# Performance work log

Hardware: AMD Instinct MI355X
Metric: run time of the kernel (lower is better)

The kernel has to match this reference:

```python
import jax, jax.numpy as jnp
import numpy as np

B, L, H = 4, 1024, 1024
NH, HD = 16, 64
ND = NH * HD
ITERS = 4
U = 5  # MSA1 ring window size (hard-coded in source)


def _conv1x1(w, b, x):  # w [O,C], b [O], x [B,C,L] -> [B,O,L]  (Conv2d 1x1 == per-position linear)
    return jnp.einsum('oc,bcl->bol', w, x) + b[None, :, None]


def _layernorm(x, s, b, eps=1e-5):  # x [B,H,L]; LayerNorm over channel dim H
    mu = x.mean(1, keepdims=True)
    var = ((x - mu) ** 2).mean(1, keepdims=True)
    return (x - mu) / jnp.sqrt(var + eps) * s[None, :, None] + b[None, :, None]


def _msa1(x, ax, wq, bq, wk, bk, wv, bv, wo, bo):
    # x [B,H,L] normalized nodes; ax [B,H,2,L] (ring embedding + relay)
    b, h, l = x.shape
    q = _conv1x1(wq, bq, x).reshape(b, NH, HD, l)
    k = _conv1x1(wk, bk, x).reshape(b, NH, HD, l)
    v = _conv1x1(wv, bv, x).reshape(b, NH, HD, l)
    pad = U // 2
    kp = jnp.pad(k, ((0, 0), (0, 0), (0, 0), (pad, pad)))
    vp = jnp.pad(v, ((0, 0), (0, 0), (0, 0), (pad, pad)))
    # F.unfold with (U,1) kernel along L == stack of U shifted views
    kw = jnp.stack([kp[..., u:u + l] for u in range(U)], axis=3)  # [B,NH,HD,U,L]
    vw = jnp.stack([vp[..., u:u + l] for u in range(U)], axis=3)
    al = ax.shape[2]
    ak = (jnp.einsum('oc,bcal->boal', wk, ax) + bk[None, :, None, None]).reshape(b, NH, HD, al, l)
    av = (jnp.einsum('oc,bcal->boal', wv, ax) + bv[None, :, None, None]).reshape(b, NH, HD, al, l)
    kw = jnp.concatenate([kw, ak], axis=3)  # [B,NH,HD,U+2,L]
    vw = jnp.concatenate([vw, av], axis=3)
    scores = (q[:, :, :, None, :] * kw).sum(2) / np.sqrt(HD)  # [B,NH,U+2,L]
    alphas = jax.nn.softmax(scores, axis=2)
    att = (alphas[:, :, None, :, :] * vw).sum(3).reshape(b, ND, l)
    return _conv1x1(wo, bo, att)  # [B,H,L]


def _msa2(relay, y, smask, wq, bq, wk, bk, wo, bo):
    # relay [B,H]; y [B,H,L+1]; smask [B,L+1] True at padding
    b = relay.shape[0]
    q = (jnp.einsum('oc,bc->bo', wq, relay) + bq).reshape(b, NH, HD)
    k = _conv1x1(wk, bk, y).reshape(b, NH, HD, -1)
    pre = jnp.einsum('bnd,bndl->bnl', q, k) / np.sqrt(HD)
    pre = jnp.where(smask[:, None, :], -1e10, pre)
    alphas = jax.nn.softmax(pre, axis=-1)
    # NOTE: source has v = k (WV output unused) -- reproduced faithfully
    att = jnp.einsum('bnl,bndl->bnd', alphas, k).reshape(b, ND)
    return jnp.einsum('oc,bc->bo', wo, att) + bo  # [B,H]


def _star_forward(data, mask, ln_s, ln_b, rwq, rwq_b, rwk, rwk_b, rwv, rwv_b, rwo, rwo_b,
                  swq, swq_b, swk, swk_b, swo, swo_b):
    b, l, h = data.shape
    pad_mask = (mask == 0)  # True at padding positions
    smask = jnp.concatenate([jnp.zeros((b, 1), bool), pad_mask], axis=1)  # [B,L+1]
    embs = jnp.transpose(data, (0, 2, 1))  # [B,H,L]
    nodes = embs
    relay = embs.mean(2)  # [B,H]
    for i in range(ITERS):
        xn = _layernorm(nodes, ln_s[i], ln_b[i])
        ax = jnp.stack([embs, jnp.broadcast_to(relay[:, :, None], embs.shape)], axis=2)  # [B,H,2,L]
        ring = _msa1(xn, ax, rwq[i], rwq_b[i], rwk[i], rwk_b[i], rwv[i], rwv_b[i], rwo[i], rwo_b[i])
        nodes = nodes + jax.nn.leaky_relu(ring)
        y = jnp.concatenate([relay[:, :, None], nodes], axis=2)  # [B,H,L+1]
        relay = jax.nn.leaky_relu(_msa2(relay, y, smask, swq[i], swq_b[i], swk[i], swk_b[i], swo[i], swo_b[i]))
        nodes = jnp.where(pad_mask[:, None, :], 0.0, nodes)
    return jnp.transpose(nodes, (0, 2, 1)), relay  # [B,L,H], [B,H]


def setup_inputs() -> dict:
    key = jax.random.key(0)
    ks = jax.random.split(key, 16)
    def p(k, shape):
        return jax.random.normal(k, shape, jnp.float32) * 0.02
    return dict(
        data=jax.random.normal(ks[0], (B, L, H), jnp.float32),
        mask=jax.random.randint(ks[1], (B, L), 0, 2).astype(jnp.int32),
        ln_s=jnp.ones((ITERS, H), jnp.float32),
        ln_b=jnp.zeros((ITERS, H), jnp.float32),
        rwq=p(ks[2], (ITERS, ND, H)), rwq_b=p(ks[3], (ITERS, ND)),
        rwk=p(ks[4], (ITERS, ND, H)), rwk_b=p(ks[5], (ITERS, ND)),
        rwv=p(ks[6], (ITERS, ND, H)), rwv_b=p(ks[7], (ITERS, ND)),
        rwo=p(ks[8], (ITERS, H, ND)), rwo_b=p(ks[9], (ITERS, H)),
        swq=p(ks[10], (ITERS, ND, H)), swq_b=p(ks[11], (ITERS, ND)),
        swk=p(ks[12], (ITERS, ND, H)), swk_b=p(ks[13], (ITERS, ND)),
        swo=p(ks[14], (ITERS, H, ND)), swo_b=p(ks[15], (ITERS, H)),
    )


def reference(data, mask, ln_s, ln_b, rwq, rwq_b, rwk, rwk_b, rwv, rwv_b, rwo, rwo_b,
              swq, swq_b, swk, swk_b, swo, swo_b):
    return _star_forward(data, mask, ln_s, ln_b, rwq, rwq_b, rwk, rwk_b, rwv, rwv_b,
                         rwo, rwo_b, swq, swq_b, swk, swk_b, swo, swo_b)
```

## Files before the change

kernel.cpp:

```cpp
#include <hip/hip_runtime.h>
#include <math.h>

namespace {

constexpr int B_ = 4, L_ = 1024, H_ = 1024, NH_ = 16, HD_ = 64, ND_ = 1024, ITERS_ = 4;

typedef unsigned short u16;
typedef __attribute__((ext_vector_type(8))) short short8;
typedef __attribute__((ext_vector_type(4))) float f32x4;

__device__ inline u16 f2bf(float f) {
  unsigned u = __builtin_bit_cast(unsigned, f);
  u += 0x7FFFu + ((u >> 16) & 1u);
  return (u16)(u >> 16);
}
__device__ inline float bf2f(u16 v) {
  unsigned u = ((unsigned)v) << 16;
  return __builtin_bit_cast(float, u);
}

__device__ inline void gl_lds16(const u16* g, u16* l) {
  __builtin_amdgcn_global_load_lds((const __attribute__((address_space(1))) void*)g,
                                   (__attribute__((address_space(3))) void*)l, 16, 0, 0);
}

__global__ void k_prep(const float* __restrict__ data, const float* __restrict__ rwq,
                       const float* __restrict__ rwk, const float* __restrict__ rwv,
                       const float* __restrict__ rwo, const float* __restrict__ swk,
                       u16* __restrict__ embs_bf, u16* __restrict__ wq_bf,
                       u16* __restrict__ wk_bf, u16* __restrict__ wv_bf,
                       u16* __restrict__ wo_bf, u16* __restrict__ swk_bf,
                       float* __restrict__ nodes) {
  int i = blockIdx.x * 256 + threadIdx.x;
  int which = blockIdx.y;
  if (which == 6) {
    reinterpret_cast<float4*>(nodes)[i] = reinterpret_cast<const float4*>(data)[i];
    return;
  }
  const float* src;
  u16* dst;
  switch (which) {
    case 0: src = data; dst = embs_bf; break;
    case 1: src = rwq; dst = wq_bf; break;
    case 2: src = rwk; dst = wk_bf; break;
    case 3: src = rwv; dst = wv_bf; break;
    case 4: src = rwo; dst = wo_bf; break;
    default: src = swk; dst = swk_bf; break;
  }
  float4 v = reinterpret_cast<const float4*>(src)[i];
  ushort4 o;
  o.x = f2bf(v.x); o.y = f2bf(v.y); o.z = f2bf(v.z); o.w = f2bf(v.w);
  reinterpret_cast<ushort4*>(dst)[i] = o;
}

__global__ void k_relay_part(const float* __restrict__ data, float* __restrict__ part) {
  int b = blockIdx.z, chunk = blockIdx.y;
  int c = blockIdx.x * 256 + threadIdx.x;
  const float* p = data + ((size_t)b * L_ + chunk * 128) * H_ + c;
  float acc = 0.f;
  for (int l = 0; l < 128; ++l) acc += p[(size_t)l * H_];
  part[((size_t)b * 8 + chunk) * H_ + c] = acc;
}
__global__ void k_relay_reduce(const float* __restrict__ part, float* __restrict__ relay) {
  int i = blockIdx.x * 256 + threadIdx.x;
  int b = i >> 10, c = i & 1023;
  float acc = 0.f;
  for (int j = 0; j < 8; ++j) acc += part[((size_t)b * 8 + j) * H_ + c];
  relay[i] = acc * (1.f / (float)L_);
}

__global__ __launch_bounds__(256) void k_layernorm_bf(float* __restrict__ nodes,
                                                      const float* __restrict__ s,
                                                      const float* __restrict__ bb,
                                                      const int* __restrict__ mask,
                                                      u16* __restrict__ y, int do_zero) {
  int row = blockIdx.x * 4 + (threadIdx.x >> 6);
  int lane = threadIdx.x & 63;
  int b = row >> 10, l = row & 1023;
  bool pad = do_zero && (mask[b * L_ + l] == 0);
  float4* xr = reinterpret_cast<float4*>(nodes + (size_t)row * H_);
  float4 v[4];
  float sum = 0.f, sq = 0.f;
#pragma unroll
  for (int j = 0; j < 4; ++j) {
    v[j] = pad ? float4{0.f, 0.f, 0.f, 0.f} : xr[lane + 64 * j];
    sum += v[j].x + v[j].y + v[j].z + v[j].w;
    sq += v[j].x * v[j].x + v[j].y * v[j].y + v[j].z * v[j].z + v[j].w * v[j].w;
  }
  if (pad) {
#pragma unroll
    for (int j = 0; j < 4; ++j) xr[lane + 64 * j] = float4{0.f, 0.f, 0.f, 0.f};
  }
#pragma unroll
  for (int off = 32; off; off >>= 1) {
    sum += __shfl_xor(sum, off);
    sq += __shfl_xor(sq, off);
  }
  float mu = sum * (1.f / (float)H_);
  float rstd = rsqrtf(sq * (1.f / (float)H_) - mu * mu + 1e-5f);
  ushort4* yr = reinterpret_cast<ushort4*>(y + (size_t)row * H_);
#pragma unroll
  for (int j = 0; j < 4; ++j) {
    int c4 = lane + 64 * j;
    float4 sc = reinterpret_cast<const float4*>(s)[c4];
    float4 bc = reinterpret_cast<const float4*>(bb)[c4];
    ushort4 o;
    o.x = f2bf((v[j].x - mu) * rstd * sc.x + bc.x);
    o.y = f2bf((v[j].y - mu) * rstd * sc.y + bc.y);
    o.z = f2bf((v[j].z - mu) * rstd * sc.z + bc.z);
    o.w = f2bf((v[j].w - mu) * rstd * sc.w + bc.w);
    yr[c4] = o;
  }
}


#define GEMM_PROLOGUE(XPTR, WPTR)                                              \
  __shared__ __align__(16) u16 sX[128 * 32];                                   \
  __shared__ __align__(16) u16 sW[128 * 32];                                   \
  const int t = threadIdx.x;                                                   \
  const int w = t >> 6, lane = t & 63;                                         \
  const int wm = w >> 1, wn = w & 1;                                           \
  const int r4 = lane >> 2, slot = lane & 3;                                   \
  const int rowS0 = w * 16 + r4, rowS1 = 64 + rowS0;                           \
  const int colS0 = ((slot ^ ((rowS0 >> 1) & 3)) << 3);                        \
  const int colS1 = ((slot ^ ((rowS1 >> 1) & 3)) << 3);                        \
  const u16* gX0 = (XPTR) + (size_t)(bm + rowS0) * 1024 + colS0;               \
  const u16* gX1 = (XPTR) + (size_t)(bm + rowS1) * 1024 + colS1;               \
  const u16* gW0 = (WPTR) + (size_t)(bn + rowS0) * 1024 + colS0;               \
  const u16* gW1 = (WPTR) + (size_t)(bn + rowS1) * 1024 + colS1;               \
  u16* lX0 = sX + (size_t)w * 512;                                             \
  u16* lX1 = sX + (size_t)(4 + w) * 512;                                       \
  u16* lW0 = sW + (size_t)w * 512;                                             \
  u16* lW1 = sW + (size_t)(4 + w) * 512;                                       \
  const int kidx = (((lane >> 4) ^ ((lane >> 1) & 3)) << 3);                   \
  f32x4 acc[4][4];                                                             \
  _Pragma("unroll") for (int i_ = 0; i_ < 4; ++i_)                             \
      _Pragma("unroll") for (int j_ = 0; j_ < 4; ++j_)                         \
          acc[i_][j_] = f32x4{0.f, 0.f, 0.f, 0.f};

#define GEMM_KLOOP(AROWBASE, BROWBASE, ASRC, BSRC)                             \
  for (int ck = 0; ck < 1024; ck += 32) {                                      \
    gl_lds16(gX0, lX0);                                                        \
    gl_lds16(gX1, lX1);                                                        \
    gl_lds16(gW0, lW0);                                                        \
    gl_lds16(gW1, lW1);                                                        \
    gX0 += 32; gX1 += 32; gW0 += 32; gW1 += 32;                                \
    __syncthreads();                                                           \
    short8 af_[4], bf_[4];                                                     \
    _Pragma("unroll") for (int mf = 0; mf < 4; ++mf)                           \
        af_[mf] = *reinterpret_cast<const short8*>(                            \
            &ASRC[((AROWBASE) + mf * 16) * 32 + kidx]);                        \
    _Pragma("unroll") for (int nf = 0; nf < 4; ++nf)                           \
        bf_[nf] = *reinterpret_cast<const short8*>(                            \
            &BSRC[((BROWBASE) + nf * 16) * 32 + kidx]);                        \
    _Pragma("unroll") for (int mf = 0; mf < 4; ++mf)                           \
        _Pragma("unroll") for (int nf = 0; nf < 4; ++nf)                       \
            acc[mf][nf] = __builtin_amdgcn_mfma_f32_16x16x32_bf16(             \
                af_[mf], bf_[nf], acc[mf][nf], 0, 0, 0);                       \
    __syncthreads();                                                          \
  }

__global__ __launch_bounds__(256) void k_gemm5(const u16* __restrict__ wq,
                                               const u16* __restrict__ wk,
                                               const u16* __restrict__ wv,
                                               const float* __restrict__ bq,
                                               const float* __restrict__ bk,
                                               const float* __restrict__ bv,
                                               const u16* __restrict__ xn,
                                               const u16* __restrict__ embs,
                                               u16* __restrict__ Y) {
  const int bm = blockIdx.x * 128;
  const int which = blockIdx.y >> 3;
  const int bn = (blockIdx.y & 7) * 128;
  const u16* W = (which == 0) ? wq : ((which == 1 || which == 3) ? wk : wv);
  const float* bias = (which == 0) ? bq : ((which == 1 || which == 3) ? bk : bv);
  const u16* X = (which < 3) ? xn : embs;
  u16* Yw = Y + (size_t)which * ((size_t)B_ * L_ * ND_);

  GEMM_PROLOGUE(X, W)
  const int rW = wm * 64 + (lane & 15);
  const int rX = wn * 64 + (lane & 15);
  GEMM_KLOOP(rW, rX, sW, sX)

#pragma unroll
  for (int mo = 0; mo < 4; ++mo) {
    int o0 = bn + wm * 64 + mo * 16 + ((lane >> 4) << 2);
    float4 bs = *reinterpret_cast<const float4*>(bias + o0);
#pragma unroll
    for (int nl = 0; nl < 4; ++nl) {
      int bl = bm + wn * 64 + nl * 16 + (lane & 15);
      f32x4 vv = acc[mo][nl];
      ushort4 ov;
      ov.x = f2bf(vv[0] + bs.x);
      ov.y = f2bf(vv[1] + bs.y);
      ov.z = f2bf(vv[2] + bs.z);
      ov.w = f2bf(vv[3] + bs.w);
      *reinterpret_cast<ushort4*>(&Yw[(size_t)bl * 1024 + o0]) = ov;
    }
  }
}

__global__ __launch_bounds__(256) void k_gemm_wo(const u16* __restrict__ W,
                                                 const float* __restrict__ bias,
                                                 const u16* __restrict__ X,
                                                 float* __restrict__ nodes,
                                                 u16* __restrict__ nodes_bf) {
  const int bm = blockIdx.x * 128;
  const int bn = blockIdx.y * 128;
  GEMM_PROLOGUE(X, W)
  const int rW = wm * 64 + (lane & 15);
  const int rX = wn * 64 + (lane & 15);
  GEMM_KLOOP(rW, rX, sW, sX)

#pragma unroll
  for (int mo = 0; mo < 4; ++mo) {
    int o0 = bn + wm * 64 + mo * 16 + ((lane >> 4) << 2);
    float4 bs = *reinterpret_cast<const float4*>(bias + o0);
#pragma unroll
    for (int nl = 0; nl < 4; ++nl) {
      int bl = bm + wn * 64 + nl * 16 + (lane & 15);
      size_t ni = (size_t)bl * 1024 + o0;
      float4 cur = *reinterpret_cast<const float4*>(&nodes[ni]);
      f32x4 vv = acc[mo][nl];
      float r0 = vv[0] + bs.x; r0 = cur.x + (r0 > 0.f ? r0 : 0.01f * r0);
      float r1 = vv[1] + bs.y; r1 = cur.y + (r1 > 0.f ? r1 : 0.01f * r1);
      float r2 = vv[2] + bs.z; r2 = cur.z + (r2 > 0.f ? r2 : 0.01f * r2);
      float r3 = vv[3] + bs.w; r3 = cur.w + (r3 > 0.f ? r3 : 0.01f * r3);
      *reinterpret_cast<float4*>(&nodes[ni]) = float4{r0, r1, r2, r3};
      ushort4 ov;
      ov.x = f2bf(r0); ov.y = f2bf(r1); ov.z = f2bf(r2); ov.w = f2bf(r3);
      *reinterpret_cast<ushort4*>(&nodes_bf[ni]) = ov;
    }
  }
}

__global__ __launch_bounds__(256) void k_gemm_kkb(const u16* __restrict__ W,
                                                  const float* __restrict__ bias,
                                                  const u16* __restrict__ X,
                                                  float* __restrict__ Y) {
  const int bm = blockIdx.x * 128;
  const int bn = blockIdx.y * 128;
  GEMM_PROLOGUE(X, W)
  const int rX = wm * 64 + (lane & 15);
  const int rW = wn * 64 + (lane & 15);
  GEMM_KLOOP(rX, rW, sX, sW)

#pragma unroll
  for (int nf = 0; nf < 4; ++nf) {
    int o = bn + wn * 64 + nf * 16 + (lane & 15);
    float bs = bias[o];
#pragma unroll
    for (int mf = 0; mf < 4; ++mf) {
      int gl = bm + wm * 64 + mf * 16 + ((lane >> 4) << 2);
      int b = gl >> 10, l = gl & 1023;
      size_t yi = ((size_t)(b * 1024 + o)) * (size_t)(L_ + 1) + 1 + l;
      f32x4 v = acc[mf][nf];
#pragma unroll
      for (int r = 0; r < 4; ++r) Y[yi + r] = v[r] + bs;
    }
  }
}

__global__ __launch_bounds__(256) void k_matvec2(const float* __restrict__ W0,
                                                 const float* __restrict__ b0,
                                                 float* __restrict__ y0, long sB0, long sO0,
                                                 const float* __restrict__ W1,
                                                 const float* __restrict__ b1,
                                                 float* __restrict__ y1, long sB1, long sO1,
                                                 const float* __restrict__ x) {
  int b = blockIdx.y;
  int z = blockIdx.z;
  const float* W = z ? W1 : W0;
  const float* bias = z ? b1 : b0;
  float* y = z ? y1 : y0;
  long sB = z ? sB1 : sB0, sO = z ? sO1 : sO0;
  int o = blockIdx.x * 4 + (threadIdx.x >> 6);
  int lane = threadIdx.x & 63;
  const float* wr = W + (size_t)o * 1024;
  const float* xb = x + (size_t)b * 1024;
  float acc = 0.f;
  for (int c = lane; c < 1024; c += 64) acc += wr[c] * xb[c];
#pragma unroll
  for (int off = 32; off; off >>= 1) acc += __shfl_xor(acc, off);
  if (lane == 0) y[(size_t)b * sB + (size_t)o * sO] = acc + bias[o];
}

__global__ __launch_bounds__(256) void k_matvec(const float* __restrict__ W,
                                                const float* __restrict__ bias,
                                                const float* __restrict__ x,
                                                float* __restrict__ y) {
  int b = blockIdx.y;
  int o = blockIdx.x * 4 + (threadIdx.x >> 6);
  int lane = threadIdx.x & 63;
  const float* wr = W + (size_t)o * 1024;
  const float* xb = x + (size_t)b * 1024;
  float acc = 0.f;
  for (int c = lane; c < 1024; c += 64) acc += wr[c] * xb[c];
#pragma unroll
  for (int off = 32; off; off >>= 1) acc += __shfl_xor(acc, off);
  if (lane == 0) {
    acc += bias[o];
    y[(size_t)b * 1024 + o] = acc > 0.f ? acc : 0.01f * acc;
  }
}

__global__ __launch_bounds__(256) void k_msa1(const u16* __restrict__ q,
                                              const u16* __restrict__ k,
                                              const u16* __restrict__ v,
                                              const u16* __restrict__ ke,
                                              const u16* __restrict__ ve,
                                              const float* __restrict__ rk,
                                              const float* __restrict__ rv,
                                              u16* __restrict__ attbf) {
  int t = threadIdx.x;
  int head = t & 15, dh = (t >> 4) & 1, lsub = t >> 5;
  int l = blockIdx.x * 8 + lsub;
  int b = blockIdx.z;
  size_t row = ((size_t)(b * 1024 + l)) * 1024 + head * 64 + dh * 32;
  size_t rbase = (size_t)b * 1024 + head * 64 + dh * 32;

  float qf[32];
  {
    const short8* qp = reinterpret_cast<const short8*>(q + row);
#pragma unroll
    for (int j = 0; j < 4; ++j) {
      short8 qv = qp[j];
#pragma unroll
      for (int e = 0; e < 8; ++e) qf[j * 8 + e] = bf2f((u16)qv[e]);
    }
  }
  float s[7];
#pragma unroll
  for (int u = 0; u < 5; ++u) {
    int lk = l + u - 2;
    float su = 0.f;
    if (lk >= 0 && lk < L_) {
      const short8* kp =
          reinterpret_cast<const short8*>(k + ((size_t)(b * 1024 + lk)) * 1024 + head * 64 + dh * 32);
#pragma unroll
      for (int j = 0; j < 4; ++j) {
        short8 kv = kp[j];
#pragma unroll
        for (int e = 0; e < 8; ++e) su = fmaf(qf[j * 8 + e], bf2f((u16)kv[e]), su);
      }
    }
    s[u] = su;
  }
  {
    float su = 0.f;
    const short8* kp = reinterpret_cast<const short8*>(ke + row);
#pragma unroll
    for (int j = 0; j < 4; ++j) {
      short8 kv = kp[j];
#pragma unroll
      for (int e = 0; e < 8; ++e) su = fmaf(qf[j * 8 + e], bf2f((u16)kv[e]), su);
    }
    s[5] = su;
  }
  {
    float su = 0.f;
    const float4* rp = reinterpret_cast<const float4*>(rk + rbase);
#pragma unroll
    for (int j = 0; j < 8; ++j) {
      float4 r4 = rp[j];
      su = fmaf(qf[j * 4 + 0], r4.x, su);
      su = fmaf(qf[j * 4 + 1], r4.y, su);
      su = fmaf(qf[j * 4 + 2], r4.z, su);
      su = fmaf(qf[j * 4 + 3], r4.w, su);
    }
    s[6] = su;
  }
#pragma unroll
  for (int u = 0; u < 7; ++u) s[u] += __shfl_xor(s[u], 16);
  float m = -1e30f;
#pragma unroll
  for (int u = 0; u < 7; ++u) {
    s[u] *= 0.125f;
    m = fmaxf(m, s[u]);
  }
  float e[7], tot = 0.f;
#pragma unroll
  for (int u = 0; u < 7; ++u) {
    e[u] = expf(s[u] - m);
    tot += e[u];
  }
  float inv = 1.f / tot;
#pragma unroll
  for (int u = 0; u < 7; ++u) e[u] *= inv;

  float av[32];
  {
    const float4* rp = reinterpret_cast<const float4*>(rv + rbase);
#pragma unroll
    for (int j = 0; j < 8; ++j) {
      float4 r4 = rp[j];
      av[j * 4 + 0] = e[6] * r4.x;
      av[j * 4 + 1] = e[6] * r4.y;
      av[j * 4 + 2] = e[6] * r4.z;
      av[j * 4 + 3] = e[6] * r4.w;
    }
  }
  {
    const short8* vp = reinterpret_cast<const short8*>(ve + row);
#pragma unroll
    for (int j = 0; j < 4; ++j) {
      short8 vv = vp[j];
#pragma unroll
      for (int ee = 0; ee < 8; ++ee) av[j * 8 + ee] = fmaf(e[5], bf2f((u16)vv[ee]), av[j * 8 + ee]);
    }
  }
#pragma unroll
  for (int u = 0; u < 5; ++u) {
    int lk = l + u - 2;
    if (lk >= 0 && lk < L_) {
      const short8* vp =
          reinterpret_cast<const short8*>(v + ((size_t)(b * 1024 + lk)) * 1024 + head * 64 + dh * 32);
#pragma unroll
      for (int j = 0; j < 4; ++j) {
        short8 vv = vp[j];
#pragma unroll
        for (int ee = 0; ee < 8; ++ee) av[j * 8 + ee] = fmaf(e[u], bf2f((u16)vv[ee]), av[j * 8 + ee]);
      }
    }
  }
  u16 ob[32];
#pragma unroll
  for (int j = 0; j < 32; ++j) ob[j] = f2bf(av[j]);
  uint4* d4 = reinterpret_cast<uint4*>(attbf + row);
  const uint4* s4 = reinterpret_cast<const uint4*>(ob);
#pragma unroll
  for (int j = 0; j < 4; ++j) d4[j] = s4[j];
}

__global__ __launch_bounds__(1024) void k_msa2(const float* __restrict__ rq,
                                               const float* __restrict__ kk,
                                               const int* __restrict__ mask,
                                               float* __restrict__ satt) {
  int n = blockIdx.x, b = blockIdx.y;
  int t = threadIdx.x;
  __shared__ float sq_[HD_];
  __shared__ float se[L_ + 1];
  __shared__ float swsum[16];
  __shared__ float stot;
  size_t rb = (size_t)(b * NH_ + n) * HD_;
  if (t < HD_) sq_[t] = rq[rb + t];
  __syncthreads();
  const float* kb = kk + rb * (size_t)(L_ + 1);
  float ls = 0.f;
  for (int p = t; p < L_ + 1; p += 1024) {
    float e;
    if (p > 0 && mask[b * L_ + p - 1] == 0) {
      e = 0.f;
    } else {
      float acc = 0.f;
      for (int d = 0; d < HD_; ++d) acc = fmaf(sq_[d], kb[(size_t)d * (L_ + 1) + p], acc);
      e = expf(acc * 0.125f);
    }
    se[p] = e;
    ls += e;
  }
  int lane = t & 63, w = t >> 6;
#pragma unroll
  for (int off = 32; off; off >>= 1) ls += __shfl_xor(ls, off);
  if (lane == 0) swsum[w] = ls;
  __syncthreads();
  if (t == 0) {
    float tot = 0.f;
    for (int j = 0; j < 16; ++j) tot += swsum[j];
    stot = 1.f / tot;
  }
  __syncthreads();
  float inv = stot;
  float acc[4] = {0.f, 0.f, 0.f, 0.f};
  const float* kw = kb + (size_t)(w * 4) * (L_ + 1);
  for (int p = lane; p < L_ + 1; p += 64) {
    float e = se[p];
#pragma unroll
    for (int j = 0; j < 4; ++j) acc[j] = fmaf(e, kw[(size_t)j * (L_ + 1) + p], acc[j]);
  }
#pragma unroll
  for (int j = 0; j < 4; ++j) {
    float a = acc[j];
#pragma unroll
    for (int off = 32; off; off >>= 1) a += __shfl_xor(a, off);
    if (lane == 0) satt[rb + w * 4 + j] = a * inv;
  }
}

__global__ void k_final(const float* __restrict__ nodes, const int* __restrict__ mask,
                        float* __restrict__ out) {
  int i = blockIdx.x * 256 + threadIdx.x;
  int row = i >> 8;
  int b = row >> 10, l = row & 1023;
  float4 v = (mask[b * L_ + l] == 0) ? float4{0.f, 0.f, 0.f, 0.f}
                                     : reinterpret_cast<const float4*>(nodes)[i];
  reinterpret_cast<float4*>(out)[i] = v;
}

__global__ void k_copy_relay(const float* __restrict__ relay, float* __restrict__ out) {
  int i = blockIdx.x * 256 + threadIdx.x;
  out[i] = relay[i];
}

}

extern "C" void kernel_launch(void* const* d_in, const int* in_sizes, int n_in,
                              void* d_out, int out_size, void* d_ws, size_t ws_size,
                              hipStream_t stream) {
  (void)in_sizes; (void)n_in; (void)out_size; (void)ws_size;
  const float* data = (const float*)d_in[0];
  const int* mask = (const int*)d_in[1];
  const float* ln_s = (const float*)d_in[2];
  const float* ln_b = (const float*)d_in[3];
  const float* rwq = (const float*)d_in[4];
  const float* rwq_b = (const float*)d_in[5];
  const float* rwk = (const float*)d_in[6];
  const float* rwk_b = (const float*)d_in[7];
  const float* rwv = (const float*)d_in[8];
  const float* rwv_b = (const float*)d_in[9];
  const float* rwo = (const float*)d_in[10];
  const float* rwo_b = (const float*)d_in[11];
  const float* swq = (const float*)d_in[12];
  const float* swq_b = (const float*)d_in[13];
  const float* swk = (const float*)d_in[14];
  const float* swk_b = (const float*)d_in[15];
  const float* swo = (const float*)d_in[16];
  const float* swo_b = (const float*)d_in[17];
  float* out = (float*)d_out;

  const size_t SZ = (size_t)B_ * ND_ * L_;
  float* f = (float*)d_ws;
  float* nodes = f; f += SZ;
  float* kkb = f; f += (size_t)B_ * ND_ * (L_ + 1);
  float* part = f; f += (size_t)B_ * 8 * H_;
  float* relay = f; f += B_ * H_;
  float* rk = f; f += B_ * ND_;
  float* rv = f; f += B_ * ND_;
  float* rq = f; f += B_ * ND_;
  float* satt = f; f += B_ * ND_;
  u16* u = (u16*)f;
  u16* xn_bf = u; u += SZ;
  u16* embs_bf = u; u += SZ;
  u16* att_bf = u; u += SZ;
  u16* nodes_bf = u; u += SZ;
  u16* qkv5_bf = u; u += 5 * SZ;
  u16* wq_bf = u; u += SZ;
  u16* wk_bf = u; u += SZ;
  u16* wv_bf = u; u += SZ;
  u16* wo_bf = u; u += SZ;
  u16* swk_bf = u; u += SZ;

  k_prep<<<dim3(4096, 7), 256, 0, stream>>>(data, rwq, rwk, rwv, rwo, swk,
                                            embs_bf, wq_bf, wk_bf, wv_bf, wo_bf, swk_bf, nodes);
  k_relay_part<<<dim3(H_ / 256, 8, B_), 256, 0, stream>>>(data, part);
  k_relay_reduce<<<dim3((B_ * H_) / 256), 256, 0, stream>>>(part, relay);

  for (int i = 0; i < ITERS_; ++i) {
    const u16* wq_i = wq_bf + (size_t)i * ND_ * H_;
    const u16* wk_i = wk_bf + (size_t)i * ND_ * H_;
    const u16* wv_i = wv_bf + (size_t)i * ND_ * H_;
    const u16* wo_i = wo_bf + (size_t)i * H_ * ND_;
    const u16* sk_i = swk_bf + (size_t)i * ND_ * H_;

    k_layernorm_bf<<<dim3(B_ * L_ / 4), 256, 0, stream>>>(nodes, ln_s + i * H_, ln_b + i * H_,
                                                          mask, xn_bf, i > 0 ? 1 : 0);
    k_gemm5<<<dim3(32, 40), 256, 0, stream>>>(wq_i, wk_i, wv_i,
                                              rwq_b + i * ND_, rwk_b + i * ND_, rwv_b + i * ND_,
                                              xn_bf, embs_bf, qkv5_bf);
    k_matvec2<<<dim3(256, B_, 2), 256, 0, stream>>>(
        rwk + (size_t)i * ND_ * H_, rwk_b + i * ND_, rk, ND_, 1,
        rwv + (size_t)i * ND_ * H_, rwv_b + i * ND_, rv, ND_, 1, relay);
    k_msa1<<<dim3(L_ / 8, 1, B_), 256, 0, stream>>>(qkv5_bf, qkv5_bf + SZ, qkv5_bf + 2 * SZ,
                                                    qkv5_bf + 3 * SZ, qkv5_bf + 4 * SZ, rk, rv, att_bf);
    k_gemm_wo<<<dim3(32, 8), 256, 0, stream>>>(wo_i, rwo_b + i * H_, att_bf, nodes, nodes_bf);
    k_matvec2<<<dim3(256, B_, 2), 256, 0, stream>>>(
        swq + (size_t)i * ND_ * H_, swq_b + i * ND_, rq, ND_, 1,
        swk + (size_t)i * ND_ * H_, swk_b + i * ND_, kkb, (long)ND_ * (L_ + 1), L_ + 1, relay);
    k_gemm_kkb<<<dim3(32, 8), 256, 0, stream>>>(sk_i, swk_b + i * ND_, nodes_bf, kkb);
    k_msa2<<<dim3(NH_, B_), 1024, 0, stream>>>(rq, kkb, mask, satt);
    k_matvec<<<dim3(256, B_), 256, 0, stream>>>(swo + (size_t)i * H_ * ND_, swo_b + i * H_, satt, relay);
  }
  k_final<<<4096, 256, 0, stream>>>(nodes, mask, out);
  k_copy_relay<<<dim3((B_ * H_) / 256), 256, 0, stream>>>(relay, out + (size_t)B_ * L_ * H_);
}
```

Baseline: 767.8 us.

## Reassociate MSA2 through WK, double K-step GEMMs, and remap MSA1 threads

MSA2 no longer materializes K = WK·nodes for all positions. It folds the query into WK (qt = WKᵀq), scores positions directly against the bf16 nodes, forms an exp-weighted sum of the nodes, and then applies WK once per head. This removes the per-iteration 1024x1024x4096 K-projection GEMM and the large kkb buffer, in exchange for several small matvec, score and sum kernels and a change in rounding order. Separately, the GEMM K loop now loads 64-wide chunks into two LDS buffers per barrier pair with a 3-block occupancy hint, and MSA1 uses 4 lanes per head so each thread holds fewer registers.

```diff
diff --git a/kernel.cpp b/kernel.cpp
--- a/kernel.cpp
+++ b/kernel.cpp
@@ -26,14 +26,13 @@
 
 __global__ void k_prep(const float* __restrict__ data, const float* __restrict__ rwq,
                        const float* __restrict__ rwk, const float* __restrict__ rwv,
-                       const float* __restrict__ rwo, const float* __restrict__ swk,
+                       const float* __restrict__ rwo,
                        u16* __restrict__ embs_bf, u16* __restrict__ wq_bf,
                        u16* __restrict__ wk_bf, u16* __restrict__ wv_bf,
-                       u16* __restrict__ wo_bf, u16* __restrict__ swk_bf,
-                       float* __restrict__ nodes) {
+                       u16* __restrict__ wo_bf, float* __restrict__ nodes) {
   int i = blockIdx.x * 256 + threadIdx.x;
   int which = blockIdx.y;
-  if (which == 6) {
+  if (which == 5) {
     reinterpret_cast<float4*>(nodes)[i] = reinterpret_cast<const float4*>(data)[i];
     return;
   }
@@ -44,8 +43,7 @@
     case 1: src = rwq; dst = wq_bf; break;
     case 2: src = rwk; dst = wk_bf; break;
     case 3: src = rwv; dst = wv_bf; break;
-    case 4: src = rwo; dst = wo_bf; break;
-    default: src = swk; dst = swk_bf; break;
+    default: src = rwo; dst = wo_bf; break;
   }
   float4 v = reinterpret_cast<const float4*>(src)[i];
   ushort4 o;
@@ -115,8 +113,8 @@
 
 
 #define GEMM_PROLOGUE(XPTR, WPTR)                                              \
-  __shared__ __align__(16) u16 sX[128 * 32];                                   \
-  __shared__ __align__(16) u16 sW[128 * 32];                                   \
+  __shared__ __align__(16) u16 sX[2][128 * 32];                                \
+  __shared__ __align__(16) u16 sW[2][128 * 32];                                \
   const int t = threadIdx.x;                                                   \
   const int w = t >> 6, lane = t & 63;                                         \
   const int wm = w >> 1, wn = w & 1;                                           \
@@ -128,47 +126,57 @@
   const u16* gX1 = (XPTR) + (size_t)(bm + rowS1) * 1024 + colS1;               \
   const u16* gW0 = (WPTR) + (size_t)(bn + rowS0) * 1024 + colS0;               \
   const u16* gW1 = (WPTR) + (size_t)(bn + rowS1) * 1024 + colS1;               \
-  u16* lX0 = sX + (size_t)w * 512;                                             \
-  u16* lX1 = sX + (size_t)(4 + w) * 512;                                       \
-  u16* lW0 = sW + (size_t)w * 512;                                             \
-  u16* lW1 = sW + (size_t)(4 + w) * 512;                                       \
+  u16* lX0a = sX[0] + w * 512;                                                 \
+  u16* lX0b = sX[1] + w * 512;                                                 \
+  u16* lX1a = sX[0] + (4 + w) * 512;                                           \
+  u16* lX1b = sX[1] + (4 + w) * 512;                                           \
+  u16* lW0a = sW[0] + w * 512;                                                 \
+  u16* lW0b = sW[1] + w * 512;                                                 \
+  u16* lW1a = sW[0] + (4 + w) * 512;                                           \
+  u16* lW1b = sW[1] + (4 + w) * 512;                                           \
   const int kidx = (((lane >> 4) ^ ((lane >> 1) & 3)) << 3);                   \
   f32x4 acc[4][4];                                                             \
   _Pragma("unroll") for (int i_ = 0; i_ < 4; ++i_)                             \
       _Pragma("unroll") for (int j_ = 0; j_ < 4; ++j_)                         \
           acc[i_][j_] = f32x4{0.f, 0.f, 0.f, 0.f};
 
-#define GEMM_KLOOP(AROWBASE, BROWBASE, ASRC, BSRC)                             \
-  for (int ck = 0; ck < 1024; ck += 32) {                                      \
-    gl_lds16(gX0, lX0);                                                        \
-    gl_lds16(gX1, lX1);                                                        \
-    gl_lds16(gW0, lW0);                                                        \
-    gl_lds16(gW1, lW1);                                                        \
-    gX0 += 32; gX1 += 32; gW0 += 32; gW1 += 32;                                \
+#define GEMM_KLOOP64(AROWBASE, BROWBASE, ASRC, BSRC)                           \
+  for (int ck = 0; ck < 1024; ck += 64) {                                      \
+    gl_lds16(gX0, lX0a);                                                       \
+    gl_lds16(gX0 + 32, lX0b);                                                  \
+    gl_lds16(gX1, lX1a);                                                       \
+    gl_lds16(gX1 + 32, lX1b);                                                  \
+    gl_lds16(gW0, lW0a);                                                       \
+    gl_lds16(gW0 + 32, lW0b);                                                  \
+    gl_lds16(gW1, lW1a);                                                       \
+    gl_lds16(gW1 + 32, lW1b);                                                  \
+    gX0 += 64; gX1 += 64; gW0 += 64; gW1 += 64;                                \
     __syncthreads();                                                           \
-    short8 af_[4], bf_[4];                                                     \
-    _Pragma("unroll") for (int mf = 0; mf < 4; ++mf)                           \
-        af_[mf] = *reinterpret_cast<const short8*>(                            \
-            &ASRC[((AROWBASE) + mf * 16) * 32 + kidx]);                        \
-    _Pragma("unroll") for (int nf = 0; nf < 4; ++nf)                           \
-        bf_[nf] = *reinterpret_cast<const short8*>(                            \
-            &BSRC[((BROWBASE) + nf * 16) * 32 + kidx]);                        \
-    _Pragma("unroll") for (int mf = 0; mf < 4; ++mf)                           \
-        _Pragma("unroll") for (int nf = 0; nf < 4; ++nf)                       \
-            acc[mf][nf] = __builtin_amdgcn_mfma_f32_16x16x32_bf16(             \
-                af_[mf], bf_[nf], acc[mf][nf], 0, 0, 0);                       \
-    __syncthreads();                                                          \
-  }
-
-__global__ __launch_bounds__(256) void k_gemm5(const u16* __restrict__ wq,
-                                               const u16* __restrict__ wk,
-                                               const u16* __restrict__ wv,
-                                               const float* __restrict__ bq,
-                                               const float* __restrict__ bk,
-                                               const float* __restrict__ bv,
-                                               const u16* __restrict__ xn,
-                                               const u16* __restrict__ embs,
-                                               u16* __restrict__ Y) {
+    _Pragma("unroll") for (int h = 0; h < 2; ++h) {                            \
+      short8 af_[4], bf_[4];                                                   \
+      _Pragma("unroll") for (int mf = 0; mf < 4; ++mf)                         \
+          af_[mf] = *reinterpret_cast<const short8*>(                          \
+              &ASRC[h][((AROWBASE) + mf * 16) * 32 + kidx]);                   \
+      _Pragma("unroll") for (int nf = 0; nf < 4; ++nf)                         \
+          bf_[nf] = *reinterpret_cast<const short8*>(                          \
+              &BSRC[h][((BROWBASE) + nf * 16) * 32 + kidx]);                   \
+      _Pragma("unroll") for (int mf = 0; mf < 4; ++mf)                         \
+          _Pragma("unroll") for (int nf = 0; nf < 4; ++nf)                     \
+              acc[mf][nf] = __builtin_amdgcn_mfma_f32_16x16x32_bf16(           \
+                  af_[mf], bf_[nf], acc[mf][nf], 0, 0, 0);                     \
+    }                                                                          \
+    __syncthreads();                                                           \
+  }
+
+__global__ __launch_bounds__(256, 3) void k_gemm5(const u16* __restrict__ wq,
+                                                  const u16* __restrict__ wk,
+                                                  const u16* __restrict__ wv,
+                                                  const float* __restrict__ bq,
+                                                  const float* __restrict__ bk,
+                                                  const float* __restrict__ bv,
+                                                  const u16* __restrict__ xn,
+                                                  const u16* __restrict__ embs,
+                                                  u16* __restrict__ Y) {
   const int bm = blockIdx.x * 128;
   const int which = blockIdx.y >> 3;
   const int bn = (blockIdx.y & 7) * 128;
@@ -180,7 +188,7 @@
   GEMM_PROLOGUE(X, W)
   const int rW = wm * 64 + (lane & 15);
   const int rX = wn * 64 + (lane & 15);
-  GEMM_KLOOP(rW, rX, sW, sX)
+  GEMM_KLOOP64(rW, rX, sW, sX)
 
 #pragma unroll
   for (int mo = 0; mo < 4; ++mo) {
@@ -200,17 +208,17 @@
   }
 }
 
-__global__ __launch_bounds__(256) void k_gemm_wo(const u16* __restrict__ W,
-                                                 const float* __restrict__ bias,
-                                                 const u16* __restrict__ X,
-                                                 float* __restrict__ nodes,
-                                                 u16* __restrict__ nodes_bf) {
+__global__ __launch_bounds__(256, 3) void k_gemm_wo(const u16* __restrict__ W,
+                                                    const float* __restrict__ bias,
+                                                    const u16* __restrict__ X,
+                                                    float* __restrict__ nodes,
+                                                    u16* __restrict__ nodes_bf) {
   const int bm = blockIdx.x * 128;
   const int bn = blockIdx.y * 128;
   GEMM_PROLOGUE(X, W)
   const int rW = wm * 64 + (lane & 15);
   const int rX = wn * 64 + (lane & 15);
-  GEMM_KLOOP(rW, rX, sW, sX)
+  GEMM_KLOOP64(rW, rX, sW, sX)
 
 #pragma unroll
   for (int mo = 0; mo < 4; ++mo) {
@@ -220,12 +228,12 @@
     for (int nl = 0; nl < 4; ++nl) {
       int bl = bm + wn * 64 + nl * 16 + (lane & 15);
       size_t ni = (size_t)bl * 1024 + o0;
-      float4 cur = *reinterpret_cast<const float4*>(&nodes[ni]);
+      float4 curv = *reinterpret_cast<const float4*>(&nodes[ni]);
       f32x4 vv = acc[mo][nl];
-      float r0 = vv[0] + bs.x; r0 = cur.x + (r0 > 0.f ? r0 : 0.01f * r0);
-      float r1 = vv[1] + bs.y; r1 = cur.y + (r1 > 0.f ? r1 : 0.01f * r1);
-      float r2 = vv[2] + bs.z; r2 = cur.z + (r2 > 0.f ? r2 : 0.01f * r2);
-      float r3 = vv[3] + bs.w; r3 = cur.w + (r3 > 0.f ? r3 : 0.01f * r3);
+      float r0 = vv[0] + bs.x; r0 = curv.x + (r0 > 0.f ? r0 : 0.01f * r0);
+      float r1 = vv[1] + bs.y; r1 = curv.y + (r1 > 0.f ? r1 : 0.01f * r1);
+      float r2 = vv[2] + bs.z; r2 = curv.z + (r2 > 0.f ? r2 : 0.01f * r2);
+      float r3 = vv[3] + bs.w; r3 = curv.w + (r3 > 0.f ? r3 : 0.01f * r3);
       *reinterpret_cast<float4*>(&nodes[ni]) = float4{r0, r1, r2, r3};
       ushort4 ov;
       ov.x = f2bf(r0); ov.y = f2bf(r1); ov.z = f2bf(r2); ov.w = f2bf(r3);
@@ -234,46 +242,18 @@
   }
 }
 
-__global__ __launch_bounds__(256) void k_gemm_kkb(const u16* __restrict__ W,
-                                                  const float* __restrict__ bias,
-                                                  const u16* __restrict__ X,
-                                                  float* __restrict__ Y) {
-  const int bm = blockIdx.x * 128;
-  const int bn = blockIdx.y * 128;
-  GEMM_PROLOGUE(X, W)
-  const int rX = wm * 64 + (lane & 15);
-  const int rW = wn * 64 + (lane & 15);
-  GEMM_KLOOP(rX, rW, sX, sW)
-
-#pragma unroll
-  for (int nf = 0; nf < 4; ++nf) {
-    int o = bn + wn * 64 + nf * 16 + (lane & 15);
-    float bs = bias[o];
-#pragma unroll
-    for (int mf = 0; mf < 4; ++mf) {
-      int gl = bm + wm * 64 + mf * 16 + ((lane >> 4) << 2);
-      int b = gl >> 10, l = gl & 1023;
-      size_t yi = ((size_t)(b * 1024 + o)) * (size_t)(L_ + 1) + 1 + l;
-      f32x4 v = acc[mf][nf];
-#pragma unroll
-      for (int r = 0; r < 4; ++r) Y[yi + r] = v[r] + bs;
-    }
-  }
-}
-
 __global__ __launch_bounds__(256) void k_matvec2(const float* __restrict__ W0,
                                                  const float* __restrict__ b0,
-                                                 float* __restrict__ y0, long sB0, long sO0,
+                                                 float* __restrict__ y0,
                                                  const float* __restrict__ W1,
                                                  const float* __restrict__ b1,
-                                                 float* __restrict__ y1, long sB1, long sO1,
+                                                 float* __restrict__ y1,
                                                  const float* __restrict__ x) {
   int b = blockIdx.y;
   int z = blockIdx.z;
   const float* W = z ? W1 : W0;
   const float* bias = z ? b1 : b0;
   float* y = z ? y1 : y0;
-  long sB = z ? sB1 : sB0, sO = z ? sO1 : sO0;
   int o = blockIdx.x * 4 + (threadIdx.x >> 6);
   int lane = threadIdx.x & 63;
   const float* wr = W + (size_t)o * 1024;
@@ -282,13 +262,13 @@
   for (int c = lane; c < 1024; c += 64) acc += wr[c] * xb[c];
 #pragma unroll
   for (int off = 32; off; off >>= 1) acc += __shfl_xor(acc, off);
-  if (lane == 0) y[(size_t)b * sB + (size_t)o * sO] = acc + bias[o];
+  if (lane == 0) y[(size_t)b * 1024 + o] = acc + bias[o];
 }
 
 __global__ __launch_bounds__(256) void k_matvec(const float* __restrict__ W,
                                                 const float* __restrict__ bias,
                                                 const float* __restrict__ x,
-                                                float* __restrict__ y) {
+                                                float* __restrict__ y, int leaky) {
   int b = blockIdx.y;
   int o = blockIdx.x * 4 + (threadIdx.x >> 6);
   int lane = threadIdx.x & 63;
@@ -300,7 +280,8 @@
   for (int off = 32; off; off >>= 1) acc += __shfl_xor(acc, off);
   if (lane == 0) {
     acc += bias[o];
-    y[(size_t)b * 1024 + o] = acc > 0.f ? acc : 0.01f * acc;
+    if (leaky) acc = acc > 0.f ? acc : 0.01f * acc;
+    y[(size_t)b * 1024 + o] = acc;
   }
 }
 
@@ -313,17 +294,18 @@
                                               const float* __restrict__ rv,
                                               u16* __restrict__ attbf) {
   int t = threadIdx.x;
-  int head = t & 15, dh = (t >> 4) & 1, lsub = t >> 5;
-  int l = blockIdx.x * 8 + lsub;
+  int wv = t >> 6, lane = t & 63;
+  int head = lane >> 2, dq = lane & 3;
+  int l = blockIdx.x * 4 + wv;
   int b = blockIdx.z;
-  size_t row = ((size_t)(b * 1024 + l)) * 1024 + head * 64 + dh * 32;
-  size_t rbase = (size_t)b * 1024 + head * 64 + dh * 32;
-
-  float qf[32];
+  size_t row = ((size_t)(b * 1024 + l)) * 1024 + head * 64 + dq * 16;
+  size_t rbase = (size_t)b * 1024 + head * 64 + dq * 16;
+
+  float qf[16];
   {
     const short8* qp = reinterpret_cast<const short8*>(q + row);
 #pragma unroll
-    for (int j = 0; j < 4; ++j) {
+    for (int j = 0; j < 2; ++j) {
       short8 qv = qp[j];
 #pragma unroll
       for (int e = 0; e < 8; ++e) qf[j * 8 + e] = bf2f((u16)qv[e]);
@@ -335,10 +317,10 @@
     int lk = l + u - 2;
     float su = 0.f;
     if (lk >= 0 && lk < L_) {
-      const short8* kp =
-          reinterpret_cast<const short8*>(k + ((size_t)(b * 1024 + lk)) * 1024 + head * 64 + dh * 32);
-#pragma unroll
-      for (int j = 0; j < 4; ++j) {
+      const short8* kp = reinterpret_cast<const short8*>(
+          k + ((size_t)(b * 1024 + lk)) * 1024 + head * 64 + dq * 16);
+#pragma unroll
+      for (int j = 0; j < 2; ++j) {
         short8 kv = kp[j];
 #pragma unroll
         for (int e = 0; e < 8; ++e) su = fmaf(qf[j * 8 + e], bf2f((u16)kv[e]), su);
@@ -350,7 +332,7 @@
     float su = 0.f;
     const short8* kp = reinterpret_cast<const short8*>(ke + row);
 #pragma unroll
-    for (int j = 0; j < 4; ++j) {
+    for (int j = 0; j < 2; ++j) {
       short8 kv = kp[j];
 #pragma unroll
       for (int e = 0; e < 8; ++e) su = fmaf(qf[j * 8 + e], bf2f((u16)kv[e]), su);
@@ -361,7 +343,7 @@
     float su = 0.f;
     const float4* rp = reinterpret_cast<const float4*>(rk + rbase);
 #pragma unroll
-    for (int j = 0; j < 8; ++j) {
+    for (int j = 0; j < 4; ++j) {
       float4 r4 = rp[j];
       su = fmaf(qf[j * 4 + 0], r4.x, su);
       su = fmaf(qf[j * 4 + 1], r4.y, su);
@@ -371,7 +353,10 @@
     s[6] = su;
   }
 #pragma unroll
-  for (int u = 0; u < 7; ++u) s[u] += __shfl_xor(s[u], 16);
+  for (int u = 0; u < 7; ++u) {
+    s[u] += __shfl_xor(s[u], 1);
+    s[u] += __shfl_xor(s[u], 2);
+  }
   float m = -1e30f;
 #pragma unroll
   for (int u = 0; u < 7; ++u) {
@@ -388,11 +373,11 @@
 #pragma unroll
   for (int u = 0; u < 7; ++u) e[u] *= inv;
 
-  float av[32];
+  float av[16];
   {
     const float4* rp = reinterpret_cast<const float4*>(rv + rbase);
 #pragma unroll
-    for (int j = 0; j < 8; ++j) {
+    for (int j = 0; j < 4; ++j) {
       float4 r4 = rp[j];
       av[j * 4 + 0] = e[6] * r4.x;
       av[j * 4 + 1] = e[6] * r4.y;
@@ -403,88 +388,129 @@
   {
     const short8* vp = reinterpret_cast<const short8*>(ve + row);
 #pragma unroll
-    for (int j = 0; j < 4; ++j) {
-      short8 vv = vp[j];
-#pragma unroll
-      for (int ee = 0; ee < 8; ++ee) av[j * 8 + ee] = fmaf(e[5], bf2f((u16)vv[ee]), av[j * 8 + ee]);
+    for (int j = 0; j < 2; ++j) {
+      short8 vvv = vp[j];
+#pragma unroll
+      for (int ee = 0; ee < 8; ++ee) av[j * 8 + ee] = fmaf(e[5], bf2f((u16)vvv[ee]), av[j * 8 + ee]);
     }
   }
 #pragma unroll
   for (int u = 0; u < 5; ++u) {
     int lk = l + u - 2;
     if (lk >= 0 && lk < L_) {
-      const short8* vp =
-          reinterpret_cast<const short8*>(v + ((size_t)(b * 1024 + lk)) * 1024 + head * 64 + dh * 32);
-#pragma unroll
-      for (int j = 0; j < 4; ++j) {
-        short8 vv = vp[j];
-#pragma unroll
-        for (int ee = 0; ee < 8; ++ee) av[j * 8 + ee] = fmaf(e[u], bf2f((u16)vv[ee]), av[j * 8 + ee]);
+      const short8* vp = reinterpret_cast<const short8*>(
+          v + ((size_t)(b * 1024 + lk)) * 1024 + head * 64 + dq * 16);
+#pragma unroll
+      for (int j = 0; j < 2; ++j) {
+        short8 vvv = vp[j];
+#pragma unroll
+        for (int ee = 0; ee < 8; ++ee) av[j * 8 + ee] = fmaf(e[u], bf2f((u16)vvv[ee]), av[j * 8 + ee]);
       }
     }
   }
-  u16 ob[32];
-#pragma unroll
-  for (int j = 0; j < 32; ++j) ob[j] = f2bf(av[j]);
+  u16 ob[16];
+#pragma unroll
+  for (int j = 0; j < 16; ++j) ob[j] = f2bf(av[j]);
   uint4* d4 = reinterpret_cast<uint4*>(attbf + row);
   const uint4* s4 = reinterpret_cast<const uint4*>(ob);
-#pragma unroll
-  for (int j = 0; j < 4; ++j) d4[j] = s4[j];
-}
-
-__global__ __launch_bounds__(1024) void k_msa2(const float* __restrict__ rq,
-                                               const float* __restrict__ kk,
+  d4[0] = s4[0];
+  d4[1] = s4[1];
+}
+
+
+__global__ __launch_bounds__(256) void k_qt(const float* __restrict__ swk,
+                                            const float* __restrict__ rq,
+                                            float* __restrict__ qt) {
+  int c = blockIdx.x * 256 + threadIdx.x;
+  int n = blockIdx.y, b = blockIdx.z;
+  __shared__ float rqs[64];
+  if (threadIdx.x < 64) rqs[threadIdx.x] = rq[(size_t)b * 1024 + n * 64 + threadIdx.x];
+  __syncthreads();
+  const float* wr = swk + (size_t)(n * 64) * 1024 + c;
+  float acc = 0.f;
+#pragma unroll 8
+  for (int d = 0; d < 64; ++d) acc = fmaf(rqs[d], wr[(size_t)d * 1024], acc);
+  qt[((size_t)b * 16 + n) * 1024 + c] = acc;
+}
+
+__global__ __launch_bounds__(256) void k_score(const float* __restrict__ qt,
+                                               const u16* __restrict__ nodes_bf,
+                                               const float* __restrict__ relay,
                                                const int* __restrict__ mask,
-                                               float* __restrict__ satt) {
-  int n = blockIdx.x, b = blockIdx.y;
-  int t = threadIdx.x;
-  __shared__ float sq_[HD_];
-  __shared__ float se[L_ + 1];
-  __shared__ float swsum[16];
-  __shared__ float stot;
-  size_t rb = (size_t)(b * NH_ + n) * HD_;
-  if (t < HD_) sq_[t] = rq[rb + t];
+                                               float* __restrict__ se,
+                                               float* __restrict__ pE) {
+  int pblk = blockIdx.x, n = blockIdx.y, b = blockIdx.z;
+  int wv = threadIdx.x >> 6, lane = threadIdx.x & 63;
+  __shared__ float qts[1024];
+  size_t bn = (size_t)b * 16 + n;
+  for (int i = threadIdx.x; i < 1024; i += 256) qts[i] = qt[bn * 1024 + i];
   __syncthreads();
-  const float* kb = kk + rb * (size_t)(L_ + 1);
-  float ls = 0.f;
-  for (int p = t; p < L_ + 1; p += 1024) {
+  float esum = 0.f;
+  for (int j = 0; j < 16; ++j) {
+    int p = pblk * 64 + wv * 16 + j;
+    if (p > 1024) break;
+    float sc = 0.f;
+    if (p == 0) {
+      const float* xr = relay + (size_t)b * 1024;
+#pragma unroll 4
+      for (int it = 0; it < 16; ++it) {
+        int c = it * 64 + lane;
+        sc = fmaf(qts[c], xr[c], sc);
+      }
+    } else {
+      const u16* xr = nodes_bf + ((size_t)b * 1024 + (p - 1)) * 1024;
+#pragma unroll 4
+      for (int it = 0; it < 16; ++it) {
+        int c = it * 64 + lane;
+        sc = fmaf(qts[c], bf2f(xr[c]), sc);
+      }
+    }
+#pragma unroll
+    for (int off = 32; off; off >>= 1) sc += __shfl_xor(sc, off);
     float e;
-    if (p > 0 && mask[b * L_ + p - 1] == 0) {
-      e = 0.f;
-    } else {
-      float acc = 0.f;
-      for (int d = 0; d < HD_; ++d) acc = fmaf(sq_[d], kb[(size_t)d * (L_ + 1) + p], acc);
-      e = expf(acc * 0.125f);
-    }
-    se[p] = e;
-    ls += e;
-  }
-  int lane = t & 63, w = t >> 6;
-#pragma unroll
-  for (int off = 32; off; off >>= 1) ls += __shfl_xor(ls, off);
-  if (lane == 0) swsum[w] = ls;
+    if (p > 0 && mask[b * L_ + p - 1] == 0) e = 0.f;
+    else e = expf(sc * 0.125f);
+    if (lane == 0) se[bn * 1025 + p] = e;
+    esum += e;
+  }
+  if (lane == 0) pE[bn * 68 + pblk * 4 + wv] = esum;
+}
+
+__global__ __launch_bounds__(256) void k_ysum(const float* __restrict__ se,
+                                              const float* __restrict__ pE,
+                                              const u16* __restrict__ nodes_bf,
+                                              const float* __restrict__ relay,
+                                              float* __restrict__ y) {
+  int cblk = blockIdx.x, n = blockIdx.y, b = blockIdx.z;
+  int c = cblk * 256 + threadIdx.x;
+  __shared__ float ses[1025];
+  size_t bn = (size_t)b * 16 + n;
+  for (int i = threadIdx.x; i < 1025; i += 256) ses[i] = se[bn * 1025 + i];
   __syncthreads();
-  if (t == 0) {
-    float tot = 0.f;
-    for (int j = 0; j < 16; ++j) tot += swsum[j];
-    stot = 1.f / tot;
-  }
-  __syncthreads();
-  float inv = stot;
-  float acc[4] = {0.f, 0.f, 0.f, 0.f};
-  const float* kw = kb + (size_t)(w * 4) * (L_ + 1);
-  for (int p = lane; p < L_ + 1; p += 64) {
-    float e = se[p];
-#pragma unroll
-    for (int j = 0; j < 4; ++j) acc[j] = fmaf(e, kw[(size_t)j * (L_ + 1) + p], acc[j]);
-  }
-#pragma unroll
-  for (int j = 0; j < 4; ++j) {
-    float a = acc[j];
-#pragma unroll
-    for (int off = 32; off; off >>= 1) a += __shfl_xor(a, off);
-    if (lane == 0) satt[rb + w * 4 + j] = a * inv;
-  }
+  float E = 0.f;
+  for (int j = 0; j < 68; ++j) E += pE[bn * 68 + j];
+  float acc = ses[0] * relay[(size_t)b * 1024 + c];
+  const u16* xc = nodes_bf + (size_t)b * 1024 * 1024 + c;
+  for (int p = 1; p <= 1024; ++p)
+    acc = fmaf(ses[p], bf2f(xc[(size_t)(p - 1) * 1024]), acc);
+  y[bn * 1024 + c] = acc / E;
+}
+
+__global__ __launch_bounds__(256) void k_att(const float* __restrict__ swk,
+                                             const float* __restrict__ bk,
+                                             const float* __restrict__ y,
+                                             float* __restrict__ satt) {
+  int b = blockIdx.y;
+  int o = blockIdx.x * 4 + (threadIdx.x >> 6);
+  int lane = threadIdx.x & 63;
+  int n = o >> 6;
+  const float* wr = swk + (size_t)o * 1024;
+  const float* yr = y + ((size_t)b * 16 + n) * 1024;
+  float acc = 0.f;
+  for (int c = lane; c < 1024; c += 64) acc = fmaf(wr[c], yr[c], acc);
+#pragma unroll
+  for (int off = 32; off; off >>= 1) acc += __shfl_xor(acc, off);
+  if (lane == 0) satt[(size_t)b * 1024 + o] = acc + bk[o];
 }
 
 __global__ void k_final(const float* __restrict__ nodes, const int* __restrict__ mask,
@@ -531,13 +557,16 @@
   const size_t SZ = (size_t)B_ * ND_ * L_;
   float* f = (float*)d_ws;
   float* nodes = f; f += SZ;
-  float* kkb = f; f += (size_t)B_ * ND_ * (L_ + 1);
   float* part = f; f += (size_t)B_ * 8 * H_;
   float* relay = f; f += B_ * H_;
   float* rk = f; f += B_ * ND_;
   float* rv = f; f += B_ * ND_;
   float* rq = f; f += B_ * ND_;
   float* satt = f; f += B_ * ND_;
+  float* qt = f; f += (size_t)B_ * 16 * 1024;
+  float* sebuf = f; f += (size_t)B_ * 16 * 1025;
+  float* pE = f; f += (size_t)B_ * 16 * 68;
+  float* ybuf = f; f += (size_t)B_ * 16 * 1024;
   u16* u = (u16*)f;
   u16* xn_bf = u; u += SZ;
   u16* embs_bf = u; u += SZ;
@@ -548,10 +577,9 @@
   u16* wk_bf = u; u += SZ;
   u16* wv_bf = u; u += SZ;
   u16* wo_bf = u; u += SZ;
-  u16* swk_bf = u; u += SZ;
-
-  k_prep<<<dim3(4096, 7), 256, 0, stream>>>(data, rwq, rwk, rwv, rwo, swk,
-                                            embs_bf, wq_bf, wk_bf, wv_bf, wo_bf, swk_bf, nodes);
+
+  k_prep<<<dim3(4096, 6), 256, 0, stream>>>(data, rwq, rwk, rwv, rwo,
+                                            embs_bf, wq_bf, wk_bf, wv_bf, wo_bf, nodes);
   k_relay_part<<<dim3(H_ / 256, 8, B_), 256, 0, stream>>>(data, part);
   k_relay_reduce<<<dim3((B_ * H_) / 256), 256, 0, stream>>>(part, relay);
 
@@ -560,7 +588,7 @@
     const u16* wk_i = wk_bf + (size_t)i * ND_ * H_;
     const u16* wv_i = wv_bf + (size_t)i * ND_ * H_;
     const u16* wo_i = wo_bf + (size_t)i * H_ * ND_;
-    const u16* sk_i = swk_bf + (size_t)i * ND_ * H_;
+    const float* swk_i = swk + (size_t)i * ND_ * H_;
 
     k_layernorm_bf<<<dim3(B_ * L_ / 4), 256, 0, stream>>>(nodes, ln_s + i * H_, ln_b + i * H_,
                                                           mask, xn_bf, i > 0 ? 1 : 0);
@@ -568,17 +596,19 @@
                                               rwq_b + i * ND_, rwk_b + i * ND_, rwv_b + i * ND_,
                                               xn_bf, embs_bf, qkv5_bf);
     k_matvec2<<<dim3(256, B_, 2), 256, 0, stream>>>(
-        rwk + (size_t)i * ND_ * H_, rwk_b + i * ND_, rk, ND_, 1,
-        rwv + (size_t)i * ND_ * H_, rwv_b + i * ND_, rv, ND_, 1, relay);
-    k_msa1<<<dim3(L_ / 8, 1, B_), 256, 0, stream>>>(qkv5_bf, qkv5_bf + SZ, qkv5_bf + 2 * SZ,
+        rwk + (size_t)i * ND_ * H_, rwk_b + i * ND_, rk,
+        rwv + (size_t)i * ND_ * H_, rwv_b + i * ND_, rv, relay);
+    k_msa1<<<dim3(L_ / 4, 1, B_), 256, 0, stream>>>(qkv5_bf, qkv5_bf + SZ, qkv5_bf + 2 * SZ,
                                                     qkv5_bf + 3 * SZ, qkv5_bf + 4 * SZ, rk, rv, att_bf);
+    k_matvec<<<dim3(256, B_), 256, 0, stream>>>(swq + (size_t)i * ND_ * H_, swq_b + i * ND_,
+                                                relay, rq, 0);
+    k_qt<<<dim3(4, NH_, B_), 256, 0, stream>>>(swk_i, rq, qt);
     k_gemm_wo<<<dim3(32, 8), 256, 0, stream>>>(wo_i, rwo_b + i * H_, att_bf, nodes, nodes_bf);
-    k_matvec2<<<dim3(256, B_, 2), 256, 0, stream>>>(
-        swq + (size_t)i * ND_ * H_, swq_b + i * ND_, rq, ND_, 1,
-        swk + (size_t)i * ND_ * H_, swk_b + i * ND_, kkb, (long)ND_ * (L_ + 1), L_ + 1, relay);
-    k_gemm_kkb<<<dim3(32, 8), 256, 0, stream>>>(sk_i, swk_b + i * ND_, nodes_bf, kkb);
-    k_msa2<<<dim3(NH_, B_), 1024, 0, stream>>>(rq, kkb, mask, satt);
-    k_matvec<<<dim3(256, B_), 256, 0, stream>>>(swo + (size_t)i * H_ * ND_, swo_b + i * H_, satt, relay);
+    k_score<<<dim3(17, NH_, B_), 256, 0, stream>>>(qt, nodes_bf, relay, mask, sebuf, pE);
+    k_ysum<<<dim3(4, NH_, B_), 256, 0, stream>>>(sebuf, pE, nodes_bf, relay, ybuf);
+    k_att<<<dim3(256, B_), 256, 0, stream>>>(swk_i, swk_b + i * ND_, ybuf, satt);
+    k_matvec<<<dim3(256, B_), 256, 0, stream>>>(swo + (size_t)i * H_ * ND_, swo_b + i * H_,
+                                                satt, relay, 1);
   }
   k_final<<<4096, 256, 0, stream>>>(nodes, mask, out);
   k_copy_relay<<<dim3((B_ * H_) / 256), 256, 0, stream>>>(relay, out + (size_t)B_ * L_ * H_);
```

New measurement: 886.8 us. 1.15x slower.
